# Performance work log

Measured on AMD Instinct MI355X. Metric: run time of the kernel, lower is better.

The kernel has to match this reference:

```python
import jax, jax.numpy as jnp
import numpy as np

SLOPE = 0.15  # LeakyReLU negative slope used throughout the module

def leaky(v):
    return jnp.where(v >= 0, v, SLOPE * v)

def _linear_params(key, fan_in, fan_out):
    kw, kb = jax.random.split(key)
    bound = 1.0 / np.sqrt(fan_in)
    W = jax.random.uniform(kw, (fan_in, fan_out), minval=-bound, maxval=bound, dtype=jnp.float32)
    b = jax.random.uniform(kb, (fan_out,), minval=-bound, maxval=bound, dtype=jnp.float32)
    return W, b

N_NODES = 50000
N_EDGES = 640000
IN_DIM = 128
EDGE_DIM = 64
HID = 128
LAT = 64

def setup_inputs() -> dict:
    key = jax.random.key(0)
    ks = jax.random.split(key, 12)
    x = jax.random.normal(ks[0], (N_NODES, IN_DIM), dtype=jnp.float32)
    edge_index = jax.random.randint(ks[1], (2, N_EDGES), 0, N_NODES, dtype=jnp.int32)
    edge_attr = jax.random.normal(ks[2], (N_EDGES, EDGE_DIM), dtype=jnp.float32)
    # conv1 params
    e1W1, e1b1 = _linear_params(ks[3], EDGE_DIM, HID)
    e1W2, e1b2 = _linear_params(ks[4], HID, HID)
    n1W, n1b = _linear_params(ks[5], IN_DIM + HID, HID)
    # conv2 params
    e2W1, e2b1 = _linear_params(ks[6], EDGE_DIM, HID)
    e2W2, e2b2 = _linear_params(ks[7], HID, HID)
    n2W, n2b = _linear_params(ks[8], HID + HID, HID)
    muW, mub = _linear_params(ks[9], HID, LAT)
    lvW, lvb = _linear_params(ks[10], HID, LAT)
    return {"x": x, "edge_index": edge_index, "edge_attr": edge_attr,
            "e1W1": e1W1, "e1b1": e1b1, "e1W2": e1W2, "e1b2": e1b2, "n1W": n1W, "n1b": n1b,
            "e2W1": e2W1, "e2b1": e2b1, "e2W2": e2W2, "e2b2": e2b2, "n2W": n2W, "n2b": n2b,
            "muW": muW, "mub": mub, "lvW": lvW, "lvb": lvb}

def edge_encoder(x, edge_index, edge_attr, eW1, eb1, eW2, eb2, nW, nb):
    # edge MLP: Linear -> LeakyReLU(0.15) -> Linear
    emb = leaky(edge_attr @ eW1 + eb1) @ eW2 + eb2           # [E, H]
    dst = edge_index[1]                                       # PyG x_i = x[target]
    z = jnp.concatenate([x[dst], emb], axis=1)                # [E, in+H]
    msg = z @ nW + nb                                         # [E, H]
    return jax.ops.segment_sum(msg, dst, num_segments=x.shape[0])  # aggr='add'

def reference(x, edge_index, edge_attr,
              e1W1, e1b1, e1W2, e1b2, n1W, n1b,
              e2W1, e2b1, e2W2, e2b2, n2W, n2b,
              muW, mub, lvW, lvb):
    # Dropout is identity in eval mode.
    h = leaky(edge_encoder(x, edge_index, edge_attr, e1W1, e1b1, e1W2, e1b2, n1W, n1b))
    h = leaky(edge_encoder(h, edge_index, edge_attr, e2W1, e2b1, e2W2, e2b2, n2W, n2b))
    mu = h @ muW + mub
    logvar = h @ lvW + lvb
    return (mu, logvar)
```

## Files before the change

kernel.cpp:

```cpp
#include <hip/hip_runtime.h>

typedef __bf16 bf16x4 __attribute__((ext_vector_type(4)));
typedef __bf16 bf16x8 __attribute__((ext_vector_type(8)));
typedef float  f32x4  __attribute__((ext_vector_type(4)));

constexpr int N_NODES = 50000;
constexpr int N_EDGES = 640000;
constexpr int NTILES  = 98;
constexpr int NB_EDGE = 2500;

__device__ __forceinline__ float leaky(float v) { return v >= 0.f ? v : 0.15f * v; }

__global__ void prep_kernel(
    const float* __restrict__ e1W1, const float* __restrict__ e1b1,
    const float* __restrict__ e1W2, const float* __restrict__ e1b2,
    const float* __restrict__ n1W,  const float* __restrict__ n1b,
    const float* __restrict__ e2W1, const float* __restrict__ e2b1,
    const float* __restrict__ e2W2, const float* __restrict__ e2b2,
    const float* __restrict__ n2W,  const float* __restrict__ n2b,
    const float* __restrict__ muW,  const float* __restrict__ mub,
    const float* __restrict__ lvW,  const float* __restrict__ lvb,
    __bf16* __restrict__ packE, __bf16* __restrict__ packN1,
    __bf16* __restrict__ packN2, __bf16* __restrict__ packH,
    float* __restrict__ ebias, float* __restrict__ c1, float* __restrict__ c2,
    float* __restrict__ hbias)
{
    int bid = blockIdx.x;
    int lane = threadIdx.x;
    int quad = lane >> 4, low = lane & 15;

    if (bid < 32) {
        int ct = bid >> 1, kt = bid & 1;
        for (int j = 0; j < 8; ++j) {
            int k = kt * 32 + quad * 8 + j;
            int n = ct * 16 + low;
            float v = (n < 128) ? e1W1[k * 128 + n] : e2W1[k * 128 + (n - 128)];
            packE[((ct * 2 + kt) * 64 + lane) * 8 + j] = (__bf16)v;
        }
    } else if (bid < 160) {
        bool is1 = bid < 96;
        int tile = bid - (is1 ? 32 : 96);
        const float* nW  = is1 ? n1W  : n2W;
        const float* eW2 = is1 ? e1W2 : e2W2;
        __bf16* dst = is1 ? packN1 : packN2;
        int ct = tile >> 3, kt = tile & 7;
        for (int j = 0; j < 8; ++j) {
            int k = kt * 32 + quad * 8 + j;
            int n = ct * 16 + low;
            float v;
            if (k < 128) {
                v = nW[k * 128 + n];
            } else {
                int i = k - 128;
                float acc = 0.f;
                for (int k2 = 0; k2 < 128; ++k2)
                    acc += eW2[i * 128 + k2] * nW[(128 + k2) * 128 + n];
                v = acc;
            }
            dst[((ct * 8 + kt) * 64 + lane) * 8 + j] = (__bf16)v;
        }
    } else if (bid < 192) {
        int tile = bid - 160;
        int ct = tile >> 2, kt = tile & 3;
        for (int j = 0; j < 8; ++j) {
            int k = kt * 32 + quad * 8 + j;
            int n = ct * 16 + low;
            float v = (n < 64) ? muW[k * 64 + n] : lvW[k * 64 + (n - 64)];
            packH[((ct * 4 + kt) * 64 + lane) * 8 + j] = (__bf16)v;
        }
    } else if (bid == 192 || bid == 193) {
        const float* nW  = (bid == 192) ? n1W  : n2W;
        const float* nb  = (bid == 192) ? n1b  : n2b;
        const float* eb2 = (bid == 192) ? e1b2 : e2b2;
        float* dst = (bid == 192) ? c1 : c2;
        for (int rep = 0; rep < 2; ++rep) {
            int j = lane + rep * 64;
            float acc = nb[j];
            for (int k = 0; k < 128; ++k)
                acc += eb2[k] * nW[(128 + k) * 128 + j];
            dst[j] = acc;
        }
    } else {
        for (int rep = 0; rep < 4; ++rep) {
            int j = lane + rep * 64;
            ebias[j] = (j < 128) ? e1b1[j] : e2b1[j - 128];
        }
        for (int rep = 0; rep < 2; ++rep) {
            int j = lane + rep * 64;
            hbias[j] = (j < 64) ? mub[j] : lvb[j - 64];
        }
    }
}

__global__ void hist_kernel(const int* __restrict__ dstp, int* __restrict__ deg) {
    int e = blockIdx.x * 256 + threadIdx.x;
    if (e < N_EDGES) atomicAdd(&deg[dstp[e]], 1);
}

__global__ void scan_a(const int* __restrict__ deg, int* __restrict__ offs,
                       int* __restrict__ tileSum, float* __restrict__ degf) {
    __shared__ int s[512];
    int t = threadIdx.x, i = blockIdx.x * 512 + t;
    int v = (i < N_NODES) ? deg[i] : 0;
    if (i < N_NODES) degf[i] = (float)v;
    s[t] = v; __syncthreads();
    for (int off = 1; off < 512; off <<= 1) {
        int x = (t >= off) ? s[t - off] : 0;
        __syncthreads();
        s[t] += x;
        __syncthreads();
    }
    if (i < N_NODES) offs[i] = s[t] - v;
    if (t == 511) tileSum[blockIdx.x] = s[511];
}

__global__ void scan_b(const int* __restrict__ tileSum, int* __restrict__ tileOff) {
    __shared__ int s[128];
    int t = threadIdx.x;
    int v = (t < NTILES) ? tileSum[t] : 0;
    s[t] = v; __syncthreads();
    for (int off = 1; off < 128; off <<= 1) {
        int x = (t >= off) ? s[t - off] : 0;
        __syncthreads();
        s[t] += x;
        __syncthreads();
    }
    if (t < NTILES) tileOff[t] = s[t] - v;
}

__global__ void scatter_kernel(const int* __restrict__ dstp, const int* __restrict__ offs,
                               const int* __restrict__ tileOff,
                               int* __restrict__ cursor, int* __restrict__ sorted,
                               int* __restrict__ sdst) {
    int e = blockIdx.x * 256 + threadIdx.x;
    if (e < N_EDGES) {
        int d = dstp[e];
        int p = offs[d] + tileOff[d >> 9] + atomicAdd(&cursor[d], 1);
        sorted[p] = e;
        sdst[p] = d;
    }
}

__global__ __launch_bounds__(256, 3) void edge_kernel(
    const float* __restrict__ edge_attr,
    const int* __restrict__ sorted, const int* __restrict__ sdst,
    const __bf16* __restrict__ packE,
    const float* __restrict__ ebias, float* __restrict__ S)
{
    __shared__ alignas(16) __bf16 Lball[4 * 64 * 72];
    __shared__ alignas(8) unsigned char runof_s[64];
    __shared__ int rundst_s[64];
    __shared__ int nruns_s;

    int tid = threadIdx.x;
    int w = tid >> 6, lane = tid & 63;
    int quad = lane >> 4, low = lane & 15;
    int r = tid >> 2, c0 = (tid & 3) * 16;

    bf16x8 bfragE[2][4];
    #pragma unroll
    for (int kt = 0; kt < 2; ++kt)
        #pragma unroll
        for (int ct = 0; ct < 4; ++ct)
            bfragE[kt][ct] = *reinterpret_cast<const bf16x8*>(
                packE + (((w * 4 + ct) * 2 + kt) * 64 + lane) * 8);
    float bias_c[4];
    #pragma unroll
    for (int ct = 0; ct < 4; ++ct) bias_c[ct] = ebias[w * 64 + ct * 16 + low];

    __bf16* As = Lball;
    __bf16* Lb = &Lball[w * 4608];

    constexpr int STRIDE = NB_EDGE * 64;
    int e0 = blockIdx.x * 64;

    float4 f0, f1, f2, f3;
    int md_c, ei_n, md_n;
    {
        int ei = sorted[e0 + r];
        md_c = sdst[e0 + lane];
        const float4* ap = reinterpret_cast<const float4*>(edge_attr + (size_t)ei * 64 + c0);
        f0 = ap[0]; f1 = ap[1]; f2 = ap[2]; f3 = ap[3];
    }
    ei_n = sorted[e0 + STRIDE + r];
    md_n = sdst[e0 + STRIDE + lane];

    #pragma unroll 1
    for (int it = 0; it < 4; ++it) {
        {
            bf16x8 v0, v1;
            v0[0]=(__bf16)f0.x; v0[1]=(__bf16)f0.y; v0[2]=(__bf16)f0.z; v0[3]=(__bf16)f0.w;
            v0[4]=(__bf16)f1.x; v0[5]=(__bf16)f1.y; v0[6]=(__bf16)f1.z; v0[7]=(__bf16)f1.w;
            v1[0]=(__bf16)f2.x; v1[1]=(__bf16)f2.y; v1[2]=(__bf16)f2.z; v1[3]=(__bf16)f2.w;
            v1[4]=(__bf16)f3.x; v1[5]=(__bf16)f3.y; v1[6]=(__bf16)f3.z; v1[7]=(__bf16)f3.w;
            *reinterpret_cast<bf16x8*>(&As[r * 72 + c0])     = v0;
            *reinterpret_cast<bf16x8*>(&As[r * 72 + c0 + 8]) = v1;
        }

        if (w == 0) {
            rundst_s[lane] = md_c;
            int dp = __shfl_up(md_c, 1);
            bool flag = (lane > 0) && (md_c != dp);
            unsigned long long mask = __ballot(flag);
            int rid = __popcll(mask & ((1ull << lane) - 1ull)) + (flag ? 1 : 0);
            runof_s[lane] = (unsigned char)rid;
            if (flag || lane == 0) rundst_s[rid] = md_c;
            if (lane == 0) nruns_s = __popcll(mask) + 1;
        }
        __syncthreads();

        float4 g0{}, g1{}, g2{}, g3{};
        if (it < 3) {
            const float4* gp = reinterpret_cast<const float4*>(
                edge_attr + (size_t)ei_n * 64 + c0);
            g0 = gp[0]; g1 = gp[1]; g2 = gp[2]; g3 = gp[3];
        }
        int ei_nn = 0, md_nn = 0;
        if (it < 2) {
            int eo = e0 + (it + 2) * STRIDE;
            ei_nn = sorted[eo + r];
            md_nn = sdst[eo + lane];
        }

        f32x4 C1[4][4] = {};
        #pragma unroll
        for (int kt = 0; kt < 2; ++kt)
            #pragma unroll
            for (int rt = 0; rt < 4; ++rt) {
                bf16x8 a = *reinterpret_cast<const bf16x8*>(
                    &As[(rt * 16 + low) * 72 + kt * 32 + quad * 8]);
                #pragma unroll
                for (int ct = 0; ct < 4; ++ct)
                    C1[rt][ct] = __builtin_amdgcn_mfma_f32_16x16x32_bf16(
                        a, bfragE[kt][ct], C1[rt][ct], 0, 0, 0);
            }
        __syncthreads();

        #pragma unroll
        for (int rt = 0; rt < 4; ++rt)
            #pragma unroll
            for (int ct = 0; ct < 4; ++ct) {
                bf16x4 v;
                #pragma unroll
                for (int rr = 0; rr < 4; ++rr)
                    v[rr] = (__bf16)leaky(C1[rt][ct][rr] + bias_c[ct]);
                *reinterpret_cast<bf16x4*>(
                    &Lb[(ct * 16 + low) * 72 + rt * 16 + quad * 4]) = v;
            }

        int nruns = nruns_s;
        for (int rt2 = 0; rt2 * 16 < nruns; ++rt2) {
            f32x4 C2[4] = {};
            #pragma unroll
            for (int kt = 0; kt < 2; ++kt) {
                uint2 rb2 = *reinterpret_cast<const uint2*>(&runof_s[kt * 32 + quad * 8]);
                unsigned target = (unsigned)(rt2 * 16 + low);
                bf16x8 a;
                #pragma unroll
                for (int j = 0; j < 8; ++j) {
                    unsigned byte = ((j < 4 ? (rb2.x >> (8 * j)) : (rb2.y >> (8 * (j - 4)))) & 0xFFu);
                    a[j] = (byte == target) ? (__bf16)1.0f : (__bf16)0.0f;
                }
                #pragma unroll
                for (int ct = 0; ct < 4; ++ct) {
                    bf16x8 b = *reinterpret_cast<const bf16x8*>(
                        &Lb[(ct * 16 + low) * 72 + kt * 32 + quad * 8]);
                    C2[ct] = __builtin_amdgcn_mfma_f32_16x16x32_bf16(a, b, C2[ct], 0, 0, 0);
                }
            }
            #pragma unroll
            for (int ct = 0; ct < 4; ++ct) {
                int col = w * 64 + ct * 16 + low;
                #pragma unroll
                for (int rr = 0; rr < 4; ++rr) {
                    int run = rt2 * 16 + quad * 4 + rr;
                    if (run < nruns) {
                        int node = rundst_s[run];
                        if ((unsigned)node < (unsigned)N_NODES)
                            unsafeAtomicAdd(&S[(size_t)node * 256 + col], C2[ct][rr]);
                    }
                }
            }
        }
        __syncthreads();

        f0 = g0; f1 = g1; f2 = g2; f3 = g3;
        md_c = md_n; ei_n = ei_nn; md_n = md_nn;
    }
}

__global__ __launch_bounds__(256) void node_fused(
    const float* __restrict__ x, const float* __restrict__ S,
    const float* __restrict__ degf,
    const __bf16* __restrict__ packN1, const __bf16* __restrict__ packN2,
    const __bf16* __restrict__ packH,
    const float* __restrict__ c1, const float* __restrict__ c2,
    const float* __restrict__ hbias,
    float* __restrict__ out)
{
    constexpr int HS = 152;
    __shared__ __bf16 Hs[4][16 * HS];
    int w = threadIdx.x >> 6, lane = threadIdx.x & 63;
    int quad = lane >> 4, low = lane & 15;
    int rb = blockIdx.x * 64 + w * 16;

    int arow = rb + low;
    if (arow >= N_NODES) arow = N_NODES - 1;
    float ds = degf[arow];
    const float* xrow = x + (size_t)arow * 128;
    const float* Srow = S + (size_t)arow * 256;

    float deg4[4];
    #pragma unroll
    for (int rr = 0; rr < 4; ++rr) {
        int row = rb + quad * 4 + rr;
        deg4[rr] = degf[row < N_NODES ? row : N_NODES - 1];
    }

    __bf16* Hw = Hs[w];

    f32x4 C[8] = {};
    #pragma unroll
    for (int kt = 0; kt < 8; ++kt) {
        const float* base = (kt < 4) ? (xrow + kt * 32 + quad * 8)
                                     : (Srow + (kt - 4) * 32 + quad * 8);
        float4 p0 = *reinterpret_cast<const float4*>(base);
        float4 p1 = *reinterpret_cast<const float4*>(base + 4);
        float m = (kt < 4) ? ds : 1.f;
        bf16x8 a;
        a[0]=(__bf16)(p0.x*m); a[1]=(__bf16)(p0.y*m); a[2]=(__bf16)(p0.z*m); a[3]=(__bf16)(p0.w*m);
        a[4]=(__bf16)(p1.x*m); a[5]=(__bf16)(p1.y*m); a[6]=(__bf16)(p1.z*m); a[7]=(__bf16)(p1.w*m);
        #pragma unroll
        for (int ct = 0; ct < 8; ++ct) {
            bf16x8 b = *reinterpret_cast<const bf16x8*>(packN1 + ((ct * 8 + kt) * 64 + lane) * 8);
            C[ct] = __builtin_amdgcn_mfma_f32_16x16x32_bf16(a, b, C[ct], 0, 0, 0);
        }
    }
    #pragma unroll
    for (int ct = 0; ct < 8; ++ct) {
        int col = ct * 16 + low;
        float cb = c1[col];
        #pragma unroll
        for (int rr = 0; rr < 4; ++rr) {
            float v = leaky(C[ct][rr] + deg4[rr] * cb);
            Hw[(quad * 4 + rr) * HS + col] = (__bf16)(v * deg4[rr]);
        }
    }

    f32x4 C2[8] = {};
    #pragma unroll
    for (int kt = 0; kt < 8; ++kt) {
        bf16x8 a;
        if (kt < 4) {
            a = *reinterpret_cast<const bf16x8*>(&Hw[low * HS + kt * 32 + quad * 8]);
        } else {
            const float* base = Srow + 128 + (kt - 4) * 32 + quad * 8;
            float4 p0 = *reinterpret_cast<const float4*>(base);
            float4 p1 = *reinterpret_cast<const float4*>(base + 4);
            a[0]=(__bf16)p0.x; a[1]=(__bf16)p0.y; a[2]=(__bf16)p0.z; a[3]=(__bf16)p0.w;
            a[4]=(__bf16)p1.x; a[5]=(__bf16)p1.y; a[6]=(__bf16)p1.z; a[7]=(__bf16)p1.w;
        }
        #pragma unroll
        for (int ct = 0; ct < 8; ++ct) {
            bf16x8 b = *reinterpret_cast<const bf16x8*>(packN2 + ((ct * 8 + kt) * 64 + lane) * 8);
            C2[ct] = __builtin_amdgcn_mfma_f32_16x16x32_bf16(a, b, C2[ct], 0, 0, 0);
        }
    }
    #pragma unroll
    for (int ct = 0; ct < 8; ++ct) {
        int col = ct * 16 + low;
        float cb = c2[col];
        #pragma unroll
        for (int rr = 0; rr < 4; ++rr) {
            float v = leaky(C2[ct][rr] + deg4[rr] * cb);
            Hw[(quad * 4 + rr) * HS + col] = (__bf16)v;
        }
    }

    f32x4 C3[8] = {};
    #pragma unroll
    for (int kt = 0; kt < 4; ++kt) {
        bf16x8 a = *reinterpret_cast<const bf16x8*>(&Hw[low * HS + kt * 32 + quad * 8]);
        #pragma unroll
        for (int ct = 0; ct < 8; ++ct) {
            bf16x8 b = *reinterpret_cast<const bf16x8*>(packH + ((ct * 4 + kt) * 64 + lane) * 8);
            C3[ct] = __builtin_amdgcn_mfma_f32_16x16x32_bf16(a, b, C3[ct], 0, 0, 0);
        }
    }
    #pragma unroll
    for (int ct = 0; ct < 8; ++ct) {
        int col = ct * 16 + low;
        float hb = hbias[col];
        #pragma unroll
        for (int rr = 0; rr < 4; ++rr) {
            int row = rb + quad * 4 + rr;
            if (row >= N_NODES) continue;
            float v = C3[ct][rr] + hb;
            if (col < 64) out[(size_t)row * 64 + col] = v;
            else          out[(size_t)N_NODES * 64 + (size_t)row * 64 + (col - 64)] = v;
        }
    }
}

extern "C" void kernel_launch(void* const* d_in, const int* in_sizes, int n_in,
                              void* d_out, int out_size, void* d_ws, size_t ws_size,
                              hipStream_t stream)
{
    const float* x     = (const float*)d_in[0];
    const int*   eidx  = (const int*)  d_in[1];
    const float* eattr = (const float*)d_in[2];
    const float* e1W1 = (const float*)d_in[3];
    const float* e1b1 = (const float*)d_in[4];
    const float* e1W2 = (const float*)d_in[5];
    const float* e1b2 = (const float*)d_in[6];
    const float* n1W  = (const float*)d_in[7];
    const float* n1b  = (const float*)d_in[8];
    const float* e2W1 = (const float*)d_in[9];
    const float* e2b1 = (const float*)d_in[10];
    const float* e2W2 = (const float*)d_in[11];
    const float* e2b2 = (const float*)d_in[12];
    const float* n2W  = (const float*)d_in[13];
    const float* n2b  = (const float*)d_in[14];
    const float* muW  = (const float*)d_in[15];
    const float* mub  = (const float*)d_in[16];
    const float* lvW  = (const float*)d_in[17];
    const float* lvb  = (const float*)d_in[18];

    const int* dstp = eidx + N_EDGES;

    char* ws = (char*)d_ws;
    size_t off = 0;
    auto alloc = [&](size_t bytes) -> void* {
        void* p = ws + off;
        off = (off + bytes + 1023) & ~(size_t)1023;
        return p;
    };
    float* S       = (float*)alloc((size_t)N_NODES * 256 * 4);
    float* h       = (float*)alloc((size_t)N_NODES * 128 * 4);
    float* g       = (float*)alloc((size_t)N_NODES * 128 * 4);
    int*   deg     = (int*)  alloc((size_t)N_NODES * 4);
    int*   cursor  = (int*)  alloc((size_t)N_NODES * 4);
    int*   offs    = (int*)  alloc((size_t)N_NODES * 4);
    float* degf    = (float*)alloc((size_t)N_NODES * 4);
    int*   sorted  = (int*)  alloc((size_t)N_EDGES * 4);
    int*   tileSum = (int*)  alloc(NTILES * 4);
    int*   tileOff = (int*)  alloc(NTILES * 4);
    __bf16* packE  = (__bf16*)alloc(32 * 64 * 8 * 2);
    __bf16* packN1 = (__bf16*)alloc(64 * 64 * 8 * 2);
    __bf16* packN2 = (__bf16*)alloc(64 * 64 * 8 * 2);
    __bf16* packH  = (__bf16*)alloc(32 * 64 * 8 * 2);
    float* ebias   = (float*)alloc(256 * 4);
    float* c1      = (float*)alloc(128 * 4);
    float* c2      = (float*)alloc(128 * 4);
    float* hbias   = (float*)alloc(128 * 4);
    (void)ws_size; (void)in_sizes; (void)n_in; (void)out_size; (void)h;

    int* sdst = (int*)g;

    hipMemsetAsync(S, 0, (size_t)N_NODES * 256 * 4, stream);
    hipMemsetAsync(deg, 0, 2 * (((size_t)N_NODES * 4 + 1023) & ~(size_t)1023), stream);

    prep_kernel<<<195, 64, 0, stream>>>(e1W1, e1b1, e1W2, e1b2, n1W, n1b,
                                        e2W1, e2b1, e2W2, e2b2, n2W, n2b,
                                        muW, mub, lvW, lvb,
                                        packE, packN1, packN2, packH,
                                        ebias, c1, c2, hbias);

    hist_kernel<<<N_EDGES / 256, 256, 0, stream>>>(dstp, deg);
    scan_a<<<NTILES, 512, 0, stream>>>(deg, offs, tileSum, degf);
    scan_b<<<1, 128, 0, stream>>>(tileSum, tileOff);
    scatter_kernel<<<N_EDGES / 256, 256, 0, stream>>>(dstp, offs, tileOff, cursor, sorted, sdst);

    edge_kernel<<<NB_EDGE, 256, 0, stream>>>(eattr, sorted, sdst, packE, ebias, S);

    node_fused<<<(N_NODES + 63) / 64, 256, 0, stream>>>(
        x, S, degf, packN1, packN2, packH, c1, c2, hbias, (float*)d_out);
}
```

Baseline: 452.1 us.

## Fuse tile-offset scan into scatter, swizzle edge LDS, compute runs in registers

The single-block scan_b kernel is removed and each scatter block recomputes the tile offsets in shared memory, saving one launch. The edge kernel drops its padded LDS layout for an XOR-swizzled one, splits the first GEMM into two halves to cut accumulator registers, and raises the occupancy hint from 3 to 4 blocks per CU. Run ids and destinations are now computed per wave with ballot/popcount, ds_permute and shuffles instead of being staged in shared memory by wave 0. These changes add redundant scan work per scatter block and more ALU for popcounts, and the higher occupancy target may force register spills.

```diff
diff --git a/kernel.cpp b/kernel.cpp
--- a/kernel.cpp
+++ b/kernel.cpp
@@ -114,49 +114,49 @@
     if (t == 511) tileSum[blockIdx.x] = s[511];
 }
 
-__global__ void scan_b(const int* __restrict__ tileSum, int* __restrict__ tileOff) {
-    __shared__ int s[128];
-    int t = threadIdx.x;
-    int v = (t < NTILES) ? tileSum[t] : 0;
-    s[t] = v; __syncthreads();
-    for (int off = 1; off < 128; off <<= 1) {
-        int x = (t >= off) ? s[t - off] : 0;
-        __syncthreads();
-        s[t] += x;
-        __syncthreads();
-    }
-    if (t < NTILES) tileOff[t] = s[t] - v;
-}
-
 __global__ void scatter_kernel(const int* __restrict__ dstp, const int* __restrict__ offs,
-                               const int* __restrict__ tileOff,
+                               const int* __restrict__ tileSum,
                                int* __restrict__ cursor, int* __restrict__ sorted,
                                int* __restrict__ sdst) {
-    int e = blockIdx.x * 256 + threadIdx.x;
+    __shared__ int s[128];
+    __shared__ int toff[128];
+    int t = threadIdx.x;
+    int v = 0;
+    if (t < 128) { v = (t < NTILES) ? tileSum[t] : 0; s[t] = v; }
+    __syncthreads();
+    for (int off = 1; off < 128; off <<= 1) {
+        int x = (t < 128 && t >= off) ? s[t - off] : 0;
+        __syncthreads();
+        if (t < 128) s[t] += x;
+        __syncthreads();
+    }
+    if (t < 128) toff[t] = s[t] - v;
+    __syncthreads();
+    int e = blockIdx.x * 256 + t;
     if (e < N_EDGES) {
         int d = dstp[e];
-        int p = offs[d] + tileOff[d >> 9] + atomicAdd(&cursor[d], 1);
+        int p = offs[d] + toff[d >> 9] + atomicAdd(&cursor[d], 1);
         sorted[p] = e;
         sdst[p] = d;
     }
 }
 
-__global__ __launch_bounds__(256, 3) void edge_kernel(
+__global__ __launch_bounds__(256, 4) void edge_kernel(
     const float* __restrict__ edge_attr,
     const int* __restrict__ sorted, const int* __restrict__ sdst,
     const __bf16* __restrict__ packE,
     const float* __restrict__ ebias, float* __restrict__ S)
 {
-    __shared__ alignas(16) __bf16 Lball[4 * 64 * 72];
-    __shared__ alignas(8) unsigned char runof_s[64];
-    __shared__ int rundst_s[64];
-    __shared__ int nruns_s;
+    __shared__ alignas(16) __bf16 As[64 * 64];
+    __shared__ alignas(16) __bf16 Lball[4 * 64 * 64];
 
     int tid = threadIdx.x;
     int w = tid >> 6, lane = tid & 63;
     int quad = lane >> 4, low = lane & 15;
     int r = tid >> 2, c0 = (tid & 3) * 16;
 
+    auto swz = [](int row, int cb) { return row * 128 + (cb ^ ((row & 7) << 4)); };
+
     bf16x8 bfragE[2][4];
     #pragma unroll
     for (int kt = 0; kt < 2; ++kt)
@@ -168,8 +168,8 @@
     #pragma unroll
     for (int ct = 0; ct < 4; ++ct) bias_c[ct] = ebias[w * 64 + ct * 16 + low];
 
-    __bf16* As = Lball;
-    __bf16* Lb = &Lball[w * 4608];
+    char* AsB = reinterpret_cast<char*>(As);
+    char* LbB = reinterpret_cast<char*>(&Lball[w * 4096]);
 
     constexpr int STRIDE = NB_EDGE * 64;
     int e0 = blockIdx.x * 64;
@@ -193,20 +193,17 @@
             v0[4]=(__bf16)f1.x; v0[5]=(__bf16)f1.y; v0[6]=(__bf16)f1.z; v0[7]=(__bf16)f1.w;
             v1[0]=(__bf16)f2.x; v1[1]=(__bf16)f2.y; v1[2]=(__bf16)f2.z; v1[3]=(__bf16)f2.w;
             v1[4]=(__bf16)f3.x; v1[5]=(__bf16)f3.y; v1[6]=(__bf16)f3.z; v1[7]=(__bf16)f3.w;
-            *reinterpret_cast<bf16x8*>(&As[r * 72 + c0])     = v0;
-            *reinterpret_cast<bf16x8*>(&As[r * 72 + c0 + 8]) = v1;
-        }
-
-        if (w == 0) {
-            rundst_s[lane] = md_c;
-            int dp = __shfl_up(md_c, 1);
-            bool flag = (lane > 0) && (md_c != dp);
-            unsigned long long mask = __ballot(flag);
-            int rid = __popcll(mask & ((1ull << lane) - 1ull)) + (flag ? 1 : 0);
-            runof_s[lane] = (unsigned char)rid;
-            if (flag || lane == 0) rundst_s[rid] = md_c;
-            if (lane == 0) nruns_s = __popcll(mask) + 1;
-        }
+            *reinterpret_cast<bf16x8*>(AsB + swz(r, c0 * 2))      = v0;
+            *reinterpret_cast<bf16x8*>(AsB + swz(r, c0 * 2 + 16)) = v1;
+        }
+
+        int dp = __shfl_up(md_c, 1);
+        bool flag = (lane > 0) && (md_c != dp);
+        unsigned long long mask = __ballot(flag);
+        int nruns = __popcll(mask) + 1;
+        int rid = __popcll(mask & ((1ull << lane) - 1ull)) + (flag ? 1 : 0);
+        int vdst = __builtin_amdgcn_ds_permute(rid << 2, md_c);
+
         __syncthreads();
 
         float4 g0{}, g1{}, g2{}, g3{};
@@ -222,66 +219,70 @@
             md_nn = sdst[eo + lane];
         }
 
-        f32x4 C1[4][4] = {};
-        #pragma unroll
-        for (int kt = 0; kt < 2; ++kt)
+        #pragma unroll
+        for (int half = 0; half < 2; ++half) {
+            f32x4 C1[2][4] = {};
             #pragma unroll
-            for (int rt = 0; rt < 4; ++rt) {
-                bf16x8 a = *reinterpret_cast<const bf16x8*>(
-                    &As[(rt * 16 + low) * 72 + kt * 32 + quad * 8]);
+            for (int kt = 0; kt < 2; ++kt)
                 #pragma unroll
-                for (int ct = 0; ct < 4; ++ct)
-                    C1[rt][ct] = __builtin_amdgcn_mfma_f32_16x16x32_bf16(
-                        a, bfragE[kt][ct], C1[rt][ct], 0, 0, 0);
-            }
-        __syncthreads();
-
-        #pragma unroll
-        for (int rt = 0; rt < 4; ++rt)
+                for (int rti = 0; rti < 2; ++rti) {
+                    int rt = half * 2 + rti;
+                    bf16x8 a = *reinterpret_cast<const bf16x8*>(
+                        AsB + swz(rt * 16 + low, kt * 64 + quad * 16));
+                    #pragma unroll
+                    for (int ct = 0; ct < 4; ++ct)
+                        C1[rti][ct] = __builtin_amdgcn_mfma_f32_16x16x32_bf16(
+                            a, bfragE[kt][ct], C1[rti][ct], 0, 0, 0);
+                }
             #pragma unroll
-            for (int ct = 0; ct < 4; ++ct) {
-                bf16x4 v;
+            for (int rti = 0; rti < 2; ++rti)
                 #pragma unroll
-                for (int rr = 0; rr < 4; ++rr)
-                    v[rr] = (__bf16)leaky(C1[rt][ct][rr] + bias_c[ct]);
-                *reinterpret_cast<bf16x4*>(
-                    &Lb[(ct * 16 + low) * 72 + rt * 16 + quad * 4]) = v;
-            }
-
-        int nruns = nruns_s;
+                for (int ct = 0; ct < 4; ++ct) {
+                    int rt = half * 2 + rti;
+                    bf16x4 v;
+                    #pragma unroll
+                    for (int rr = 0; rr < 4; ++rr)
+                        v[rr] = (__bf16)leaky(C1[rti][ct][rr] + bias_c[ct]);
+                    *reinterpret_cast<bf16x4*>(
+                        LbB + swz(ct * 16 + low, rt * 32 + quad * 8)) = v;
+                }
+        }
+
         for (int rt2 = 0; rt2 * 16 < nruns; ++rt2) {
+            int target = rt2 * 16 + low;
             f32x4 C2[4] = {};
             #pragma unroll
             for (int kt = 0; kt < 2; ++kt) {
-                uint2 rb2 = *reinterpret_cast<const uint2*>(&runof_s[kt * 32 + quad * 8]);
-                unsigned target = (unsigned)(rt2 * 16 + low);
+                int bsh = 63 - kt * 32 - quad * 8;
                 bf16x8 a;
                 #pragma unroll
                 for (int j = 0; j < 8; ++j) {
-                    unsigned byte = ((j < 4 ? (rb2.x >> (8 * j)) : (rb2.y >> (8 * (j - 4)))) & 0xFFu);
-                    a[j] = (byte == target) ? (__bf16)1.0f : (__bf16)0.0f;
+                    int ride = __popcll(mask << (bsh - j));
+                    a[j] = (ride == target) ? (__bf16)1.0f : (__bf16)0.0f;
                 }
                 #pragma unroll
                 for (int ct = 0; ct < 4; ++ct) {
                     bf16x8 b = *reinterpret_cast<const bf16x8*>(
-                        &Lb[(ct * 16 + low) * 72 + kt * 32 + quad * 8]);
+                        LbB + swz(ct * 16 + low, kt * 64 + quad * 16));
                     C2[ct] = __builtin_amdgcn_mfma_f32_16x16x32_bf16(a, b, C2[ct], 0, 0, 0);
                 }
             }
+            int node4[4];
+            #pragma unroll
+            for (int rr = 0; rr < 4; ++rr)
+                node4[rr] = __shfl(vdst, rt2 * 16 + quad * 4 + rr);
             #pragma unroll
             for (int ct = 0; ct < 4; ++ct) {
                 int col = w * 64 + ct * 16 + low;
                 #pragma unroll
                 for (int rr = 0; rr < 4; ++rr) {
                     int run = rt2 * 16 + quad * 4 + rr;
-                    if (run < nruns) {
-                        int node = rundst_s[run];
-                        if ((unsigned)node < (unsigned)N_NODES)
-                            unsafeAtomicAdd(&S[(size_t)node * 256 + col], C2[ct][rr]);
-                    }
+                    if (run < nruns && (unsigned)node4[rr] < (unsigned)N_NODES)
+                        unsafeAtomicAdd(&S[(size_t)node4[rr] * 256 + col], C2[ct][rr]);
                 }
             }
         }
+
         __syncthreads();
 
         f0 = g0; f1 = g1; f2 = g2; f3 = g3;
@@ -444,7 +445,6 @@
     float* degf    = (float*)alloc((size_t)N_NODES * 4);
     int*   sorted  = (int*)  alloc((size_t)N_EDGES * 4);
     int*   tileSum = (int*)  alloc(NTILES * 4);
-    int*   tileOff = (int*)  alloc(NTILES * 4);
     __bf16* packE  = (__bf16*)alloc(32 * 64 * 8 * 2);
     __bf16* packN1 = (__bf16*)alloc(64 * 64 * 8 * 2);
     __bf16* packN2 = (__bf16*)alloc(64 * 64 * 8 * 2);
@@ -468,8 +468,7 @@
 
     hist_kernel<<<N_EDGES / 256, 256, 0, stream>>>(dstp, deg);
     scan_a<<<NTILES, 512, 0, stream>>>(deg, offs, tileSum, degf);
-    scan_b<<<1, 128, 0, stream>>>(tileSum, tileOff);
-    scatter_kernel<<<N_EDGES / 256, 256, 0, stream>>>(dstp, offs, tileOff, cursor, sorted, sdst);
+    scatter_kernel<<<N_EDGES / 256, 256, 0, stream>>>(dstp, offs, tileSum, cursor, sorted, sdst);
 
     edge_kernel<<<NB_EDGE, 256, 0, stream>>>(eattr, sorted, sdst, packE, ebias, S);
 
```

Result: slower. 629.4 us (+39.2%).
